# Kernel optimization log

Hardware: AMD Instinct MI355X
Metric: run time of the kernel (lower is better)

The kernel has to match this reference:

```python
import jax, jax.numpy as jnp
import numpy as np


def gcn_conv(x, src, dst, norm, W, b, n_nodes):
    # PyG GCNConv: out[dst] = sum_edges norm * (x @ W)[src] + b
    h = x @ W                      # [N, F_out]
    msg = h[src] * norm[:, None]   # [E', F_out] gather + scale
    out = jax.ops.segment_sum(msg, dst, num_segments=n_nodes)
    return out + b


def _gcn_norm(edge_index, n_nodes):
    # add self loops, compute symmetric normalization deg^-1/2[src]*deg^-1/2[dst]
    loop = jnp.arange(n_nodes, dtype=edge_index.dtype)
    src = jnp.concatenate([edge_index[0], loop])
    dst = jnp.concatenate([edge_index[1], loop])
    deg = jnp.zeros((n_nodes,), jnp.float32).at[dst].add(1.0)
    dinv = jnp.where(deg > 0, jax.lax.rsqrt(deg), 0.0)
    norm = dinv[src] * dinv[dst]
    return src, dst, norm


def setup_inputs() -> dict:
    key = jax.random.key(0)
    ks = jax.random.split(key, 5)
    N, E, C_in, C_out = 50000, 800000, 128, 32
    H = 2 * C_out
    x = jax.random.normal(ks[0], (N, C_in), jnp.float32)
    edge_index = jax.random.randint(ks[1], (2, E), 0, N, jnp.int64)
    s1 = 1.0 / np.sqrt(C_in)
    s2 = 1.0 / np.sqrt(H)
    W1 = jax.random.uniform(ks[2], (C_in, H), jnp.float32, -s1, s1)
    b1 = jnp.zeros((H,), jnp.float32)
    W_mu = jax.random.uniform(ks[3], (H, C_out), jnp.float32, -s2, s2)
    b_mu = jnp.zeros((C_out,), jnp.float32)
    W_ls = jax.random.uniform(ks[4], (H, C_out), jnp.float32, -s2, s2)
    b_ls = jnp.zeros((C_out,), jnp.float32)
    return {"x": x, "edge_index": edge_index, "W1": W1, "b1": b1,
            "W_mu": W_mu, "b_mu": b_mu, "W_ls": W_ls, "b_ls": b_ls}


def reference(x, edge_index, W1, b1, W_mu, b_mu, W_ls, b_ls):
    n_nodes = x.shape[0]
    src, dst, norm = _gcn_norm(edge_index, n_nodes)
    h = jax.nn.relu(gcn_conv(x, src, dst, norm, W1, b1, n_nodes))
    mu = gcn_conv(h, src, dst, norm, W_mu, b_mu, n_nodes)
    logstd = gcn_conv(h, src, dst, norm, W_ls, b_ls, n_nodes)
    return mu, logstd
```

## Files before the change

### kernel.cpp

```cpp
#include <hip/hip_runtime.h>
#include <hip/hip_fp16.h>
#include <math.h>


typedef unsigned int uint;
typedef unsigned short ushort;
typedef __attribute__((ext_vector_type(8))) short short8;
typedef __attribute__((ext_vector_type(4))) float f32x4;

#define CAPC 48
#define CAPB 5120

__device__ __forceinline__ ushort f2bf(float x) {
    uint u = __float_as_uint(x);
    u += 0x7fffu + ((u >> 16) & 1u);
    return (ushort)(u >> 16);
}
__device__ __forceinline__ float bf2f(ushort h) {
    return __uint_as_float((uint)h << 16);
}

__global__ __launch_bounds__(256) void k_scatter(
        const int* __restrict__ src, const int* __restrict__ dst,
        int* __restrict__ cmat, uint* __restrict__ recs, int E, int SB) {
    __shared__ int h[256];
    const int tid = threadIdx.x;
    const int bx  = blockIdx.x;
    h[tid] = 0;
    __syncthreads();
    const int base = bx * 2048;
    uint rec[8]; int rk[8];
    #pragma unroll
    for (int k = 0; k < 8; ++k) {
        int i = base + k * 256 + tid;
        if (i < E) {
            int s = __builtin_nontemporal_load(src + i);
            int d = __builtin_nontemporal_load(dst + i);
            int b = d >> 8;
            rec[k] = (uint)s | ((uint)(d & 255) << 16) | ((uint)b << 24);
            rk[k] = atomicAdd(&h[b], 1);
        }
    }
    __syncthreads();
    cmat[bx * 256 + tid] = h[tid];
    #pragma unroll
    for (int k = 0; k < 8; ++k) {
        int i = base + k * 256 + tid;
        if (i < E) {
            int b = rec[k] >> 24;
            if (rk[k] < CAPC)
                recs[((size_t)b * SB + bx) * CAPC + rk[k]] = rec[k];
        }
    }
}

__global__ __launch_bounds__(256, 4) void k_phaseB(
        const uint* __restrict__ recs, const int* __restrict__ cmat,
        int* __restrict__ rp2, float* __restrict__ dinv,
        ushort* __restrict__ edges, int N, int NBUCK, int SB) {
    __shared__ int h[256];
    __shared__ int p[256];
    __shared__ int cc[512];
    __shared__ int co[512];
    __shared__ int lowTot, scnt;
    __shared__ uint rstage[CAPB];
    const int tid = threadIdx.x;
    const int bx  = blockIdx.x;
    h[tid] = 0;
    cc[tid]       = (tid < SB)       ? min(cmat[tid * 256 + bx], CAPC) : 0;
    cc[tid + 256] = (tid + 256 < SB) ? min(cmat[(tid + 256) * 256 + bx], CAPC) : 0;
    __syncthreads();
    int v = cc[tid];
    p[tid] = v;
    __syncthreads();
    #pragma unroll
    for (int off = 1; off < 256; off <<= 1) {
        int xv = (tid >= off) ? p[tid - off] : 0;
        __syncthreads();
        p[tid] += xv;
        __syncthreads();
    }
    co[tid] = p[tid] - v;
    if (tid == 255) lowTot = p[255];
    __syncthreads();
    v = cc[tid + 256];
    p[tid] = v;
    __syncthreads();
    #pragma unroll
    for (int off = 1; off < 256; off <<= 1) {
        int xv = (tid >= off) ? p[tid - off] : 0;
        __syncthreads();
        p[tid] += xv;
        __syncthreads();
    }
    co[tid + 256] = p[tid] - v + lowTot;
    if (tid == 255) scnt = lowTot + p[255];
    __syncthreads();
    const int TOTS4 = SB * (CAPC / 4);
    for (int s4 = tid; s4 < TOTS4; s4 += 256) {
        const int sb = s4 / (CAPC / 4);
        const int i0 = (s4 - sb * (CAPC / 4)) * 4;
        const int c  = cc[sb];
        if (i0 < c) {
            const uint4 r4 = *(const uint4*)(recs +
                                 ((size_t)bx * SB + sb) * CAPC + i0);
            const int d0 = co[sb] + i0;
            const int nv = min(c - i0, 4);
            uint rr[4] = {r4.x, r4.y, r4.z, r4.w};
            #pragma unroll
            for (int j = 0; j < 4; ++j) {
                if (j < nv && d0 + j < CAPB) {
                    rstage[d0 + j] = rr[j];
                    atomicAdd(&h[(rr[j] >> 16) & 255], 1);
                }
            }
        }
    }
    __syncthreads();
    v = h[tid];
    p[tid] = v;
    __syncthreads();
    #pragma unroll
    for (int off = 1; off < 256; off <<= 1) {
        int xv = (tid >= off) ? p[tid - off] : 0;
        __syncthreads();
        p[tid] += xv;
        __syncthreads();
    }
    const int excl = p[tid] - v;
    const int node = bx * 256 + tid;
    rp2[bx * 257 + tid] = bx * CAPB + excl;
    if (tid == 255) rp2[bx * 257 + 256] = bx * CAPB + excl + v;
    if (node < N) dinv[node] = rsqrtf((float)(v + 1));
    h[tid] = excl;
    __syncthreads();
    const int cnt = min(scnt, CAPB);
    for (int i = tid; i < cnt; i += 256) {
        uint r = rstage[i];
        int pos = atomicAdd(&h[(r >> 16) & 255], 1);
        if (pos < CAPB)
            edges[(size_t)bx * CAPB + pos] = (ushort)(r & 0xffffu);
    }
}

__global__ __launch_bounds__(256, 4) void k_gemm(
        const float* __restrict__ x, const float* __restrict__ W1,
        const float* __restrict__ dinv, ushort* __restrict__ hp, int N) {
    __shared__ ushort Wt[64][136];
    const int tid = threadIdx.x;
    #pragma unroll
    for (int it = 0; it < 8; ++it) {
        int idx = (it * 256 + tid) * 4;
        int k = idx >> 6, c = idx & 63;
        float4 wv = *(const float4*)(W1 + idx);
        Wt[c + 0][k] = f2bf(wv.x);
        Wt[c + 1][k] = f2bf(wv.y);
        Wt[c + 2][k] = f2bf(wv.z);
        Wt[c + 3][k] = f2bf(wv.w);
    }
    __syncthreads();
    const int w = tid >> 6, l = tid & 63;
    const int m = l & 15, q = l >> 4;
    const int row0 = blockIdx.x * 64 + w * 16;
    const size_t arow = (size_t)min(row0 + m, N - 1);
    f32x4 acc0 = {0.f, 0.f, 0.f, 0.f}, acc1 = acc0, acc2 = acc0, acc3 = acc0;
    #pragma unroll
    for (int kc = 0; kc < 4; ++kc) {
        const int kofs = kc * 32 + q * 8;
        const float4* xr = (const float4*)(x + arow * 128 + kofs);
        float4 xa = xr[0], xb = xr[1];
        short8 a;
        a[0] = (short)f2bf(xa.x); a[1] = (short)f2bf(xa.y);
        a[2] = (short)f2bf(xa.z); a[3] = (short)f2bf(xa.w);
        a[4] = (short)f2bf(xb.x); a[5] = (short)f2bf(xb.y);
        a[6] = (short)f2bf(xb.z); a[7] = (short)f2bf(xb.w);
        short8 b0 = *(const short8*)&Wt[m][kofs];
        short8 b1 = *(const short8*)&Wt[m + 16][kofs];
        short8 b2 = *(const short8*)&Wt[m + 32][kofs];
        short8 b3 = *(const short8*)&Wt[m + 48][kofs];
        acc0 = __builtin_amdgcn_mfma_f32_16x16x32_bf16(a, b0, acc0, 0, 0, 0);
        acc1 = __builtin_amdgcn_mfma_f32_16x16x32_bf16(a, b1, acc1, 0, 0, 0);
        acc2 = __builtin_amdgcn_mfma_f32_16x16x32_bf16(a, b2, acc2, 0, 0, 0);
        acc3 = __builtin_amdgcn_mfma_f32_16x16x32_bf16(a, b3, acc3, 0, 0, 0);
    }
    #pragma unroll
    for (int r = 0; r < 4; ++r) {
        int row = row0 + q * 4 + r;
        if (row >= N) continue;
        float dv = dinv[row];
        ushort* hr = hp + (size_t)row * 64 + m;
        hr[0]  = f2bf(acc0[r] * dv);
        hr[16] = f2bf(acc1[r] * dv);
        hr[32] = f2bf(acc2[r] * dv);
        hr[48] = f2bf(acc3[r] * dv);
    }
}

__device__ __forceinline__ void gather_grp8(
        const uint* __restrict__ hp, const ushort* __restrict__ edges,
        int beg, int end, int ECAP, int sl, float4& a0, float4& a1) {
    for (int base = beg; base < end; base += 8) {
        const int mrec = (int)edges[min(base + sl, ECAP - 1)];
        const int cnt = end - base;
        if (cnt >= 8) {
            #pragma unroll
            for (int i = 0; i < 8; ++i) {
                const int r = __shfl(mrec, i, 8);
                const uint4 v = *(const uint4*)(hp + (size_t)r * 32 + 4 * sl);
                a0.x += __uint_as_float(v.x << 16);
                a0.y += __uint_as_float(v.x & 0xffff0000u);
                a0.z += __uint_as_float(v.y << 16);
                a0.w += __uint_as_float(v.y & 0xffff0000u);
                a1.x += __uint_as_float(v.z << 16);
                a1.y += __uint_as_float(v.z & 0xffff0000u);
                a1.z += __uint_as_float(v.w << 16);
                a1.w += __uint_as_float(v.w & 0xffff0000u);
            }
        } else {
            #pragma unroll
            for (int i = 0; i < 7; ++i) {
                const int r = __shfl(mrec, min(i, cnt - 1), 8);
                uint4 v = *(const uint4*)(hp + (size_t)r * 32 + 4 * sl);
                if (i >= cnt) { v.x = 0u; v.y = 0u; v.z = 0u; v.w = 0u; }
                a0.x += __uint_as_float(v.x << 16);
                a0.y += __uint_as_float(v.x & 0xffff0000u);
                a0.z += __uint_as_float(v.y << 16);
                a0.w += __uint_as_float(v.y & 0xffff0000u);
                a1.x += __uint_as_float(v.z << 16);
                a1.y += __uint_as_float(v.z & 0xffff0000u);
                a1.z += __uint_as_float(v.w << 16);
                a1.w += __uint_as_float(v.w & 0xffff0000u);
            }
        }
    }
}

__global__ __launch_bounds__(256, 6) void k_gather1(
        const uint* __restrict__ hp, const int* __restrict__ rp2,
        const ushort* __restrict__ edges, const float* __restrict__ dinv,
        const float* __restrict__ b1, uint* __restrict__ ho, int N, int ECAP) {
    const int lane = threadIdx.x & 63;
    const int sl = lane & 7;
    const int n = blockIdx.x * 32 + ((threadIdx.x >> 6) << 3) + (lane >> 3);
    const int nc = min(n, N - 1);
    const int beg = rp2[(nc >> 8) * 257 + (nc & 255)];
    const int end = rp2[(nc >> 8) * 257 + (nc & 255) + 1];
    float4 a0 = {0.f, 0.f, 0.f, 0.f}, a1 = a0;
    gather_grp8(hp, edges, beg, end, ECAP, sl, a0, a1);
    const float dv = dinv[nc];
    const uint4 sv = *(const uint4*)(hp + (size_t)nc * 32 + 4 * sl);
    const float4 bA = ((const float4*)b1)[2 * sl];
    const float4 bB = ((const float4*)b1)[2 * sl + 1];
    float s0 = a0.x + bf2f((ushort)sv.x);
    float s1 = a0.y + bf2f((ushort)(sv.x >> 16));
    float s2 = a0.z + bf2f((ushort)sv.y);
    float s3 = a0.w + bf2f((ushort)(sv.y >> 16));
    float s4 = a1.x + bf2f((ushort)sv.z);
    float s5 = a1.y + bf2f((ushort)(sv.z >> 16));
    float s6 = a1.z + bf2f((ushort)sv.w);
    float s7 = a1.w + bf2f((ushort)(sv.w >> 16));
    float h0 = fmaxf(fmaf(dv, s0, bA.x), 0.f) * dv;
    float h1 = fmaxf(fmaf(dv, s1, bA.y), 0.f) * dv;
    float h2 = fmaxf(fmaf(dv, s2, bA.z), 0.f) * dv;
    float h3 = fmaxf(fmaf(dv, s3, bA.w), 0.f) * dv;
    float h4 = fmaxf(fmaf(dv, s4, bB.x), 0.f) * dv;
    float h5 = fmaxf(fmaf(dv, s5, bB.y), 0.f) * dv;
    float h6 = fmaxf(fmaf(dv, s6, bB.z), 0.f) * dv;
    float h7 = fmaxf(fmaf(dv, s7, bB.w), 0.f) * dv;
    if (n < N) {
        uint4 o;
        o.x = (uint)f2bf(h0) | ((uint)f2bf(h1) << 16);
        o.y = (uint)f2bf(h2) | ((uint)f2bf(h3) << 16);
        o.z = (uint)f2bf(h4) | ((uint)f2bf(h5) << 16);
        o.w = (uint)f2bf(h6) | ((uint)f2bf(h7) << 16);
        *(uint4*)(ho + (size_t)n * 32 + 4 * sl) = o;
    }
}

__global__ __launch_bounds__(256, 6) void k_gather2(
        const uint* __restrict__ hp, const int* __restrict__ rp2,
        const ushort* __restrict__ edges, const float* __restrict__ dinv,
        const float* __restrict__ Wmu, const float* __restrict__ Wls,
        const float* __restrict__ bmu, const float* __restrict__ bls,
        float* __restrict__ out, int N, int ECAP) {
    __shared__ __align__(16) float hs[4][8][64];
    const int lane = threadIdx.x & 63;
    const int sl = lane & 7, grp = lane >> 3;
    const int w = threadIdx.x >> 6;
    const int n = blockIdx.x * 32 + (w << 3) + grp;
    const int nc = min(n, N - 1);
    const int beg = rp2[(nc >> 8) * 257 + (nc & 255)];
    const int end = rp2[(nc >> 8) * 257 + (nc & 255) + 1];
    float4 a0 = {0.f, 0.f, 0.f, 0.f}, a1 = a0;
    gather_grp8(hp, edges, beg, end, ECAP, sl, a0, a1);
    const float dv = dinv[nc];
    const uint4 sv = *(const uint4*)(hp + (size_t)nc * 32 + 4 * sl);
    float4 gA, gB;
    gA.x = dv * (a0.x + bf2f((ushort)sv.x));
    gA.y = dv * (a0.y + bf2f((ushort)(sv.x >> 16)));
    gA.z = dv * (a0.z + bf2f((ushort)sv.y));
    gA.w = dv * (a0.w + bf2f((ushort)(sv.y >> 16)));
    gB.x = dv * (a1.x + bf2f((ushort)sv.z));
    gB.y = dv * (a1.y + bf2f((ushort)(sv.z >> 16)));
    gB.z = dv * (a1.z + bf2f((ushort)sv.w));
    gB.w = dv * (a1.w + bf2f((ushort)(sv.w >> 16)));
    *(float4*)&hs[w][grp][8 * sl]     = gA;
    *(float4*)&hs[w][grp][8 * sl + 4] = gB;
    const float* Wsel = (lane < 32) ? (Wmu + lane) : (Wls + (lane - 32));
    const float bias  = (lane < 32) ? bmu[lane] : bls[lane - 32];
    #pragma unroll
    for (int p = 0; p < 2; ++p) {
        float c0 = 0.f, c1 = 0.f, c2 = 0.f, c3 = 0.f;
        #pragma unroll 4
        for (int k = 0; k < 64; ++k) {
            float wv = Wsel[k * 32];
            c0 = fmaf(hs[w][p * 4 + 0][k], wv, c0);
            c1 = fmaf(hs[w][p * 4 + 1][k], wv, c1);
            c2 = fmaf(hs[w][p * 4 + 2][k], wv, c2);
            c3 = fmaf(hs[w][p * 4 + 3][k], wv, c3);
        }
        const int n0 = blockIdx.x * 32 + (w << 3) + p * 4;
        float cs[4] = {c0, c1, c2, c3};
        #pragma unroll
        for (int gg = 0; gg < 4; ++gg) {
            int nn = n0 + gg;
            if (nn >= N) break;
            float t = cs[gg] + bias;
            if (lane < 32) out[(size_t)nn * 32 + lane] = t;
            else           out[(size_t)N * 32 + (size_t)nn * 32 + (lane - 32)] = t;
        }
    }
}

extern "C" void kernel_launch(void* const* d_in, const int* in_sizes, int n_in,
                              void* d_out, int out_size, void* d_ws, size_t ws_size,
                              hipStream_t stream) {
    const float* x   = (const float*)d_in[0];
    const int*   ei  = (const int*)d_in[1];
    const float* W1  = (const float*)d_in[2];
    const float* b1  = (const float*)d_in[3];
    const float* Wmu = (const float*)d_in[4];
    const float* bmu = (const float*)d_in[5];
    const float* Wls = (const float*)d_in[6];
    const float* bls = (const float*)d_in[7];
    float* out = (float*)d_out;

    const int N = in_sizes[0] / 128;
    const int E = in_sizes[1] / 2;
    const int* src = ei;
    const int* dst = ei + E;
    const int SB    = (E + 2047) / 2048;
    const int NBUCK = (N + 255) / 256;
    const int GB    = (N + 63) / 64;
    const int NG    = (N + 31) / 32;
    const int ECAP  = NBUCK * CAPB;

    char* w = (char*)d_ws;
    auto carve = [&](size_t bytes) { char* p = w; w += (bytes + 1023) & ~(size_t)1023; return p; };
    int*    cmat    = (int*)   carve((size_t)SB * 256 * 4);
    uint*   recs    = (uint*)  carve((size_t)NBUCK * SB * CAPC * 4);
    int*    rp2     = (int*)   carve((size_t)NBUCK * 257 * 4);
    float*  dinv    = (float*) carve((size_t)N * 4);
    ushort* edges   = (ushort*)carve((size_t)ECAP * 2);
    ushort* h_pre   = (ushort*)carve((size_t)N * 64 * 2);
    ushort* h_mid   = (ushort*)carve((size_t)N * 64 * 2);

    k_scatter <<<SB, 256, 0, stream>>>(src, dst, cmat, recs, E, SB);
    k_phaseB  <<<NBUCK, 256, 0, stream>>>(recs, cmat, rp2, dinv, edges,
                                          N, NBUCK, SB);
    k_gemm    <<<GB, 256, 0, stream>>>(x, W1, dinv, h_pre, N);
    k_gather1 <<<NG, 256, 0, stream>>>((const uint*)h_pre, rp2, edges, dinv,
                                       b1, (uint*)h_mid, N, ECAP);
    k_gather2 <<<NG, 256, 0, stream>>>((const uint*)h_mid, rp2, edges, dinv,
                                       Wmu, Wls, bmu, bls, out, N, ECAP);
}
```

Before: 167.7 us.

## Fuse edge scatter with feature GEMM and move source normalization into gathers

The GEMM no longer depends on the degree-normalization vector, so its blocks are merged into the edge-scatter launch. Both run concurrently, which saves one kernel launch and lets the GEMM overlap the scatter. To make that possible, the per-source dinv scaling is no longer applied to stored features and is instead loaded per edge inside the gather loops, using an FMA in place of the add. This adds an extra random 4-byte load per edge in both gather passes, and the fused kernel now carries the GEMM's shared-memory footprint for every block.

```diff
diff --git a/kernel.cpp b/kernel.cpp
--- a/kernel.cpp
+++ b/kernel.cpp
@@ -20,36 +20,88 @@
     return __uint_as_float((uint)h << 16);
 }
 
-__global__ __launch_bounds__(256) void k_scatter(
-        const int* __restrict__ src, const int* __restrict__ dst,
-        int* __restrict__ cmat, uint* __restrict__ recs, int E, int SB) {
+__global__ __launch_bounds__(256, 4) void k_scatgemm(
+        const int* __restrict__ srcp, const int* __restrict__ dstp,
+        int* __restrict__ cmat, uint* __restrict__ recs,
+        const float* __restrict__ x, const float* __restrict__ W1,
+        ushort* __restrict__ hp, int E, int SB, int N) {
     __shared__ int h[256];
+    __shared__ ushort Wt[64][136];
     const int tid = threadIdx.x;
-    const int bx  = blockIdx.x;
-    h[tid] = 0;
-    __syncthreads();
-    const int base = bx * 2048;
-    uint rec[8]; int rk[8];
-    #pragma unroll
-    for (int k = 0; k < 8; ++k) {
-        int i = base + k * 256 + tid;
-        if (i < E) {
-            int s = __builtin_nontemporal_load(src + i);
-            int d = __builtin_nontemporal_load(dst + i);
-            int b = d >> 8;
-            rec[k] = (uint)s | ((uint)(d & 255) << 16) | ((uint)b << 24);
-            rk[k] = atomicAdd(&h[b], 1);
-        }
-    }
-    __syncthreads();
-    cmat[bx * 256 + tid] = h[tid];
-    #pragma unroll
-    for (int k = 0; k < 8; ++k) {
-        int i = base + k * 256 + tid;
-        if (i < E) {
-            int b = rec[k] >> 24;
-            if (rk[k] < CAPC)
-                recs[((size_t)b * SB + bx) * CAPC + rk[k]] = rec[k];
+    if ((int)blockIdx.x < SB) {
+        const int bx = blockIdx.x;
+        h[tid] = 0;
+        __syncthreads();
+        const int base = bx * 2048;
+        uint rec[8]; int rk[8];
+        #pragma unroll
+        for (int k = 0; k < 8; ++k) {
+            int i = base + k * 256 + tid;
+            if (i < E) {
+                int s = __builtin_nontemporal_load(srcp + i);
+                int d = __builtin_nontemporal_load(dstp + i);
+                int b = d >> 8;
+                rec[k] = (uint)s | ((uint)(d & 255) << 16) | ((uint)b << 24);
+                rk[k] = atomicAdd(&h[b], 1);
+            }
+        }
+        __syncthreads();
+        cmat[bx * 256 + tid] = h[tid];
+        #pragma unroll
+        for (int k = 0; k < 8; ++k) {
+            int i = base + k * 256 + tid;
+            if (i < E) {
+                int b = rec[k] >> 24;
+                if (rk[k] < CAPC)
+                    recs[((size_t)b * SB + bx) * CAPC + rk[k]] = rec[k];
+            }
+        }
+    } else {
+        const int bx = blockIdx.x - SB;
+        #pragma unroll
+        for (int it = 0; it < 8; ++it) {
+            int idx = (it * 256 + tid) * 4;
+            int k = idx >> 6, c = idx & 63;
+            float4 wv = *(const float4*)(W1 + idx);
+            Wt[c + 0][k] = f2bf(wv.x);
+            Wt[c + 1][k] = f2bf(wv.y);
+            Wt[c + 2][k] = f2bf(wv.z);
+            Wt[c + 3][k] = f2bf(wv.w);
+        }
+        __syncthreads();
+        const int w = tid >> 6, l = tid & 63;
+        const int m = l & 15, q = l >> 4;
+        const int row0 = bx * 64 + w * 16;
+        const size_t arow = (size_t)min(row0 + m, N - 1);
+        f32x4 acc0 = {0.f, 0.f, 0.f, 0.f}, acc1 = acc0, acc2 = acc0, acc3 = acc0;
+        #pragma unroll
+        for (int kc = 0; kc < 4; ++kc) {
+            const int kofs = kc * 32 + q * 8;
+            const float4* xr = (const float4*)(x + arow * 128 + kofs);
+            float4 xa = xr[0], xb = xr[1];
+            short8 a;
+            a[0] = (short)f2bf(xa.x); a[1] = (short)f2bf(xa.y);
+            a[2] = (short)f2bf(xa.z); a[3] = (short)f2bf(xa.w);
+            a[4] = (short)f2bf(xb.x); a[5] = (short)f2bf(xb.y);
+            a[6] = (short)f2bf(xb.z); a[7] = (short)f2bf(xb.w);
+            short8 b0 = *(const short8*)&Wt[m][kofs];
+            short8 b1 = *(const short8*)&Wt[m + 16][kofs];
+            short8 b2 = *(const short8*)&Wt[m + 32][kofs];
+            short8 b3 = *(const short8*)&Wt[m + 48][kofs];
+            acc0 = __builtin_amdgcn_mfma_f32_16x16x32_bf16(a, b0, acc0, 0, 0, 0);
+            acc1 = __builtin_amdgcn_mfma_f32_16x16x32_bf16(a, b1, acc1, 0, 0, 0);
+            acc2 = __builtin_amdgcn_mfma_f32_16x16x32_bf16(a, b2, acc2, 0, 0, 0);
+            acc3 = __builtin_amdgcn_mfma_f32_16x16x32_bf16(a, b3, acc3, 0, 0, 0);
+        }
+        #pragma unroll
+        for (int r = 0; r < 4; ++r) {
+            int row = row0 + q * 4 + r;
+            if (row >= N) continue;
+            ushort* hr = hp + (size_t)row * 64 + m;
+            hr[0]  = f2bf(acc0[r]);
+            hr[16] = f2bf(acc1[r]);
+            hr[32] = f2bf(acc2[r]);
+            hr[48] = f2bf(acc3[r]);
         }
     }
 }
@@ -143,62 +195,10 @@
     }
 }
 
-__global__ __launch_bounds__(256, 4) void k_gemm(
-        const float* __restrict__ x, const float* __restrict__ W1,
-        const float* __restrict__ dinv, ushort* __restrict__ hp, int N) {
-    __shared__ ushort Wt[64][136];
-    const int tid = threadIdx.x;
-    #pragma unroll
-    for (int it = 0; it < 8; ++it) {
-        int idx = (it * 256 + tid) * 4;
-        int k = idx >> 6, c = idx & 63;
-        float4 wv = *(const float4*)(W1 + idx);
-        Wt[c + 0][k] = f2bf(wv.x);
-        Wt[c + 1][k] = f2bf(wv.y);
-        Wt[c + 2][k] = f2bf(wv.z);
-        Wt[c + 3][k] = f2bf(wv.w);
-    }
-    __syncthreads();
-    const int w = tid >> 6, l = tid & 63;
-    const int m = l & 15, q = l >> 4;
-    const int row0 = blockIdx.x * 64 + w * 16;
-    const size_t arow = (size_t)min(row0 + m, N - 1);
-    f32x4 acc0 = {0.f, 0.f, 0.f, 0.f}, acc1 = acc0, acc2 = acc0, acc3 = acc0;
-    #pragma unroll
-    for (int kc = 0; kc < 4; ++kc) {
-        const int kofs = kc * 32 + q * 8;
-        const float4* xr = (const float4*)(x + arow * 128 + kofs);
-        float4 xa = xr[0], xb = xr[1];
-        short8 a;
-        a[0] = (short)f2bf(xa.x); a[1] = (short)f2bf(xa.y);
-        a[2] = (short)f2bf(xa.z); a[3] = (short)f2bf(xa.w);
-        a[4] = (short)f2bf(xb.x); a[5] = (short)f2bf(xb.y);
-        a[6] = (short)f2bf(xb.z); a[7] = (short)f2bf(xb.w);
-        short8 b0 = *(const short8*)&Wt[m][kofs];
-        short8 b1 = *(const short8*)&Wt[m + 16][kofs];
-        short8 b2 = *(const short8*)&Wt[m + 32][kofs];
-        short8 b3 = *(const short8*)&Wt[m + 48][kofs];
-        acc0 = __builtin_amdgcn_mfma_f32_16x16x32_bf16(a, b0, acc0, 0, 0, 0);
-        acc1 = __builtin_amdgcn_mfma_f32_16x16x32_bf16(a, b1, acc1, 0, 0, 0);
-        acc2 = __builtin_amdgcn_mfma_f32_16x16x32_bf16(a, b2, acc2, 0, 0, 0);
-        acc3 = __builtin_amdgcn_mfma_f32_16x16x32_bf16(a, b3, acc3, 0, 0, 0);
-    }
-    #pragma unroll
-    for (int r = 0; r < 4; ++r) {
-        int row = row0 + q * 4 + r;
-        if (row >= N) continue;
-        float dv = dinv[row];
-        ushort* hr = hp + (size_t)row * 64 + m;
-        hr[0]  = f2bf(acc0[r] * dv);
-        hr[16] = f2bf(acc1[r] * dv);
-        hr[32] = f2bf(acc2[r] * dv);
-        hr[48] = f2bf(acc3[r] * dv);
-    }
-}
-
 __device__ __forceinline__ void gather_grp8(
         const uint* __restrict__ hp, const ushort* __restrict__ edges,
-        int beg, int end, int ECAP, int sl, float4& a0, float4& a1) {
+        const float* __restrict__ dinv, int beg, int end, int ECAP, int sl,
+        float4& a0, float4& a1) {
     for (int base = beg; base < end; base += 8) {
         const int mrec = (int)edges[min(base + sl, ECAP - 1)];
         const int cnt = end - base;
@@ -206,30 +206,32 @@
             #pragma unroll
             for (int i = 0; i < 8; ++i) {
                 const int r = __shfl(mrec, i, 8);
+                const float dvs = dinv[r];
                 const uint4 v = *(const uint4*)(hp + (size_t)r * 32 + 4 * sl);
-                a0.x += __uint_as_float(v.x << 16);
-                a0.y += __uint_as_float(v.x & 0xffff0000u);
-                a0.z += __uint_as_float(v.y << 16);
-                a0.w += __uint_as_float(v.y & 0xffff0000u);
-                a1.x += __uint_as_float(v.z << 16);
-                a1.y += __uint_as_float(v.z & 0xffff0000u);
-                a1.z += __uint_as_float(v.w << 16);
-                a1.w += __uint_as_float(v.w & 0xffff0000u);
+                a0.x = fmaf(__uint_as_float(v.x << 16),          dvs, a0.x);
+                a0.y = fmaf(__uint_as_float(v.x & 0xffff0000u),  dvs, a0.y);
+                a0.z = fmaf(__uint_as_float(v.y << 16),          dvs, a0.z);
+                a0.w = fmaf(__uint_as_float(v.y & 0xffff0000u),  dvs, a0.w);
+                a1.x = fmaf(__uint_as_float(v.z << 16),          dvs, a1.x);
+                a1.y = fmaf(__uint_as_float(v.z & 0xffff0000u),  dvs, a1.y);
+                a1.z = fmaf(__uint_as_float(v.w << 16),          dvs, a1.z);
+                a1.w = fmaf(__uint_as_float(v.w & 0xffff0000u),  dvs, a1.w);
             }
         } else {
             #pragma unroll
             for (int i = 0; i < 7; ++i) {
                 const int r = __shfl(mrec, min(i, cnt - 1), 8);
+                const float dvs = dinv[r];
                 uint4 v = *(const uint4*)(hp + (size_t)r * 32 + 4 * sl);
                 if (i >= cnt) { v.x = 0u; v.y = 0u; v.z = 0u; v.w = 0u; }
-                a0.x += __uint_as_float(v.x << 16);
-                a0.y += __uint_as_float(v.x & 0xffff0000u);
-                a0.z += __uint_as_float(v.y << 16);
-                a0.w += __uint_as_float(v.y & 0xffff0000u);
-                a1.x += __uint_as_float(v.z << 16);
-                a1.y += __uint_as_float(v.z & 0xffff0000u);
-                a1.z += __uint_as_float(v.w << 16);
-                a1.w += __uint_as_float(v.w & 0xffff0000u);
+                a0.x = fmaf(__uint_as_float(v.x << 16),          dvs, a0.x);
+                a0.y = fmaf(__uint_as_float(v.x & 0xffff0000u),  dvs, a0.y);
+                a0.z = fmaf(__uint_as_float(v.y << 16),          dvs, a0.z);
+                a0.w = fmaf(__uint_as_float(v.y & 0xffff0000u),  dvs, a0.w);
+                a1.x = fmaf(__uint_as_float(v.z << 16),          dvs, a1.x);
+                a1.y = fmaf(__uint_as_float(v.z & 0xffff0000u),  dvs, a1.y);
+                a1.z = fmaf(__uint_as_float(v.w << 16),          dvs, a1.z);
+                a1.w = fmaf(__uint_as_float(v.w & 0xffff0000u),  dvs, a1.w);
             }
         }
     }
@@ -246,27 +248,27 @@
     const int beg = rp2[(nc >> 8) * 257 + (nc & 255)];
     const int end = rp2[(nc >> 8) * 257 + (nc & 255) + 1];
     float4 a0 = {0.f, 0.f, 0.f, 0.f}, a1 = a0;
-    gather_grp8(hp, edges, beg, end, ECAP, sl, a0, a1);
+    gather_grp8(hp, edges, dinv, beg, end, ECAP, sl, a0, a1);
     const float dv = dinv[nc];
     const uint4 sv = *(const uint4*)(hp + (size_t)nc * 32 + 4 * sl);
     const float4 bA = ((const float4*)b1)[2 * sl];
     const float4 bB = ((const float4*)b1)[2 * sl + 1];
-    float s0 = a0.x + bf2f((ushort)sv.x);
-    float s1 = a0.y + bf2f((ushort)(sv.x >> 16));
-    float s2 = a0.z + bf2f((ushort)sv.y);
-    float s3 = a0.w + bf2f((ushort)(sv.y >> 16));
-    float s4 = a1.x + bf2f((ushort)sv.z);
-    float s5 = a1.y + bf2f((ushort)(sv.z >> 16));
-    float s6 = a1.z + bf2f((ushort)sv.w);
-    float s7 = a1.w + bf2f((ushort)(sv.w >> 16));
-    float h0 = fmaxf(fmaf(dv, s0, bA.x), 0.f) * dv;
-    float h1 = fmaxf(fmaf(dv, s1, bA.y), 0.f) * dv;
-    float h2 = fmaxf(fmaf(dv, s2, bA.z), 0.f) * dv;
-    float h3 = fmaxf(fmaf(dv, s3, bA.w), 0.f) * dv;
-    float h4 = fmaxf(fmaf(dv, s4, bB.x), 0.f) * dv;
-    float h5 = fmaxf(fmaf(dv, s5, bB.y), 0.f) * dv;
-    float h6 = fmaxf(fmaf(dv, s6, bB.z), 0.f) * dv;
-    float h7 = fmaxf(fmaf(dv, s7, bB.w), 0.f) * dv;
+    float s0 = a0.x + dv * bf2f((ushort)sv.x);
+    float s1 = a0.y + dv * bf2f((ushort)(sv.x >> 16));
+    float s2 = a0.z + dv * bf2f((ushort)sv.y);
+    float s3 = a0.w + dv * bf2f((ushort)(sv.y >> 16));
+    float s4 = a1.x + dv * bf2f((ushort)sv.z);
+    float s5 = a1.y + dv * bf2f((ushort)(sv.z >> 16));
+    float s6 = a1.z + dv * bf2f((ushort)sv.w);
+    float s7 = a1.w + dv * bf2f((ushort)(sv.w >> 16));
+    float h0 = fmaxf(fmaf(dv, s0, bA.x), 0.f);
+    float h1 = fmaxf(fmaf(dv, s1, bA.y), 0.f);
+    float h2 = fmaxf(fmaf(dv, s2, bA.z), 0.f);
+    float h3 = fmaxf(fmaf(dv, s3, bA.w), 0.f);
+    float h4 = fmaxf(fmaf(dv, s4, bB.x), 0.f);
+    float h5 = fmaxf(fmaf(dv, s5, bB.y), 0.f);
+    float h6 = fmaxf(fmaf(dv, s6, bB.z), 0.f);
+    float h7 = fmaxf(fmaf(dv, s7, bB.w), 0.f);
     if (n < N) {
         uint4 o;
         o.x = (uint)f2bf(h0) | ((uint)f2bf(h1) << 16);
@@ -292,18 +294,18 @@
     const int beg = rp2[(nc >> 8) * 257 + (nc & 255)];
     const int end = rp2[(nc >> 8) * 257 + (nc & 255) + 1];
     float4 a0 = {0.f, 0.f, 0.f, 0.f}, a1 = a0;
-    gather_grp8(hp, edges, beg, end, ECAP, sl, a0, a1);
+    gather_grp8(hp, edges, dinv, beg, end, ECAP, sl, a0, a1);
     const float dv = dinv[nc];
     const uint4 sv = *(const uint4*)(hp + (size_t)nc * 32 + 4 * sl);
     float4 gA, gB;
-    gA.x = dv * (a0.x + bf2f((ushort)sv.x));
-    gA.y = dv * (a0.y + bf2f((ushort)(sv.x >> 16)));
-    gA.z = dv * (a0.z + bf2f((ushort)sv.y));
-    gA.w = dv * (a0.w + bf2f((ushort)(sv.y >> 16)));
-    gB.x = dv * (a1.x + bf2f((ushort)sv.z));
-    gB.y = dv * (a1.y + bf2f((ushort)(sv.z >> 16)));
-    gB.z = dv * (a1.z + bf2f((ushort)sv.w));
-    gB.w = dv * (a1.w + bf2f((ushort)(sv.w >> 16)));
+    gA.x = dv * (a0.x + dv * bf2f((ushort)sv.x));
+    gA.y = dv * (a0.y + dv * bf2f((ushort)(sv.x >> 16)));
+    gA.z = dv * (a0.z + dv * bf2f((ushort)sv.y));
+    gA.w = dv * (a0.w + dv * bf2f((ushort)(sv.y >> 16)));
+    gB.x = dv * (a1.x + dv * bf2f((ushort)sv.z));
+    gB.y = dv * (a1.y + dv * bf2f((ushort)(sv.z >> 16)));
+    gB.z = dv * (a1.z + dv * bf2f((ushort)sv.w));
+    gB.w = dv * (a1.w + dv * bf2f((ushort)(sv.w >> 16)));
     *(float4*)&hs[w][grp][8 * sl]     = gA;
     *(float4*)&hs[w][grp][8 * sl + 4] = gB;
     const float* Wsel = (lane < 32) ? (Wmu + lane) : (Wls + (lane - 32));
@@ -365,10 +367,10 @@
     ushort* h_pre   = (ushort*)carve((size_t)N * 64 * 2);
     ushort* h_mid   = (ushort*)carve((size_t)N * 64 * 2);
 
-    k_scatter <<<SB, 256, 0, stream>>>(src, dst, cmat, recs, E, SB);
+    k_scatgemm<<<SB + GB, 256, 0, stream>>>(src, dst, cmat, recs,
+                                            x, W1, h_pre, E, SB, N);
     k_phaseB  <<<NBUCK, 256, 0, stream>>>(recs, cmat, rp2, dinv, edges,
                                           N, NBUCK, SB);
-    k_gemm    <<<GB, 256, 0, stream>>>(x, W1, dinv, h_pre, N);
     k_gather1 <<<NG, 256, 0, stream>>>((const uint*)h_pre, rp2, edges, dinv,
                                        b1, (uint*)h_mid, N, ECAP);
     k_gather2 <<<NG, 256, 0, stream>>>((const uint*)h_mid, rp2, edges, dinv,
```

Result: slower. 178.4 us (+6.4%).
